# Kernel tuning notes

Measured on AMD Instinct MI355X. Metric: run time of the kernel, lower is better.

Reference implementation:

```python
import jax, jax.numpy as jnp
import numpy as np

N = 32768       # total nodes = NUM_GRAPHS * T
F_IN = 32       # num_features
HC = 64         # hidden_channels
HEADS = 4
E = 524288      # edges before self-loops
NUM_GRAPHS = 64 # == batch.max()+1 by construction
T = 512         # time steps per graph (N // NUM_GRAPHS)
OUT = 24        # output_size
NEG_SLOPE = 0.2 # PyG GATConv default


def gat_layer(x, src, dst, W, a_src, a_dst, b, n_nodes):
    """PyG GATConv (concat=True) with edge softmax over incoming edges."""
    H, C = a_src.shape
    h = (x @ W).reshape(n_nodes, H, C)                    # [N,H,C]
    alpha_src = jnp.sum(h * a_src, axis=-1)               # [N,H]
    alpha_dst = jnp.sum(h * a_dst, axis=-1)               # [N,H]
    e = jax.nn.leaky_relu(alpha_src[src] + alpha_dst[dst], NEG_SLOPE)  # [E,H]
    m = jax.ops.segment_max(e, dst, num_segments=n_nodes)
    e = jnp.exp(e - m[dst])
    s = jax.ops.segment_sum(e, dst, num_segments=n_nodes)
    alpha = e / (s[dst] + 1e-16)                          # [E,H]
    msg = h[src] * alpha[..., None]                       # [E,H,C]
    out = jax.ops.segment_sum(msg, dst, num_segments=n_nodes)  # [N,H,C]
    return out.reshape(n_nodes, H * C) + b


def gru_layer(x, Wih, Whh, bih, bhh):
    """torch nn.GRU single layer, batch_first input x: [B,T,Hin] -> ([B,T,H], h_T)."""
    Bsz = x.shape[0]
    H = Whh.shape[1]

    def step(h, xt):
        gi = xt @ Wih.T + bih
        gh = h @ Whh.T + bhh
        ir, iz, inn = jnp.split(gi, 3, axis=-1)
        hr, hz, hn = jnp.split(gh, 3, axis=-1)
        r = jax.nn.sigmoid(ir + hr)
        z = jax.nn.sigmoid(iz + hz)
        n = jnp.tanh(inn + r * hn)
        h_new = (1.0 - z) * n + z * h
        return h_new, h_new

    h0 = jnp.zeros((Bsz, H), x.dtype)
    hT, ys = jax.lax.scan(step, h0, jnp.swapaxes(x, 0, 1))
    return jnp.swapaxes(ys, 0, 1), hT


def setup_inputs() -> dict:
    key = jax.random.key(0)
    ks = jax.random.split(key, 24)
    sc = 0.1
    inp = {
        "x": jax.random.normal(ks[0], (N, F_IN), dtype=jnp.float32),
        "edge_index": jax.random.randint(ks[1], (2, E), 0, N, dtype=jnp.int32),
        "batch": jnp.repeat(jnp.arange(NUM_GRAPHS, dtype=jnp.int32), T),
        # GAT layer 1: F_IN -> HC x HEADS (concat)
        "W1": sc * jax.random.normal(ks[2], (F_IN, HEADS * HC), dtype=jnp.float32),
        "a_src1": sc * jax.random.normal(ks[3], (HEADS, HC), dtype=jnp.float32),
        "a_dst1": sc * jax.random.normal(ks[4], (HEADS, HC), dtype=jnp.float32),
        "b1": jnp.zeros((HEADS * HC,), dtype=jnp.float32),
        # GAT layer 2: HEADS*HC -> HC, 1 head
        "W2": sc * jax.random.normal(ks[5], (HEADS * HC, HC), dtype=jnp.float32),
        "a_src2": sc * jax.random.normal(ks[6], (1, HC), dtype=jnp.float32),
        "a_dst2": sc * jax.random.normal(ks[7], (1, HC), dtype=jnp.float32),
        "b2": jnp.zeros((HC,), dtype=jnp.float32),
        # GRU (2 layers, input_size == hidden_size == HC)
        "gru_Wih0": sc * jax.random.normal(ks[8], (3 * HC, HC), dtype=jnp.float32),
        "gru_Whh0": sc * jax.random.normal(ks[9], (3 * HC, HC), dtype=jnp.float32),
        "gru_bih0": jnp.zeros((3 * HC,), dtype=jnp.float32),
        "gru_bhh0": jnp.zeros((3 * HC,), dtype=jnp.float32),
        "gru_Wih1": sc * jax.random.normal(ks[10], (3 * HC, HC), dtype=jnp.float32),
        "gru_Whh1": sc * jax.random.normal(ks[11], (3 * HC, HC), dtype=jnp.float32),
        "gru_bih1": jnp.zeros((3 * HC,), dtype=jnp.float32),
        "gru_bhh1": jnp.zeros((3 * HC,), dtype=jnp.float32),
        # Linear head
        "Wl": sc * jax.random.normal(ks[12], (OUT, HC), dtype=jnp.float32),
        "bl": jnp.zeros((OUT,), dtype=jnp.float32),
    }
    return inp


def reference(x, edge_index, batch, W1, a_src1, a_dst1, b1, W2, a_src2, a_dst2, b2,
              gru_Wih0, gru_Whh0, gru_bih0, gru_bhh0,
              gru_Wih1, gru_Whh1, gru_bih1, gru_bhh1, Wl, bl):
    # PyG GATConv default add_self_loops=True
    loops = jnp.arange(N, dtype=edge_index.dtype)
    src = jnp.concatenate([edge_index[0], loops])
    dst = jnp.concatenate([edge_index[1], loops])

    h = jax.nn.elu(gat_layer(x, src, dst, W1, a_src1, a_dst1, b1, N))   # [N, HEADS*HC]
    h = jax.nn.elu(gat_layer(h, src, dst, W2, a_src2, a_dst2, b2, N))   # [N, HC]

    # batch is repeat(arange(NUM_GRAPHS), T) so batch.max()+1 == NUM_GRAPHS (static)
    seq = h.reshape(NUM_GRAPHS, T, HC)
    seq, _ = gru_layer(seq, gru_Wih0, gru_Whh0, gru_bih0, gru_bhh0)
    _, hT = gru_layer(seq, gru_Wih1, gru_Whh1, gru_bih1, gru_bhh1)      # [B, HC]
    return hT @ Wl.T + bl                                               # [B, OUT]
```

## Files before the change

kernel.cpp:

```cpp
#include <hip/hip_runtime.h>
#include <hip/hip_bf16.h>

#define N_NODES 32768
#define F_IN    32
#define HC      64
#define HEADS   4
#define NE      524288
#define NET     (NE + N_NODES)
#define NG      64
#define TT      512
#define OUTF    24

__device__ __forceinline__ float lrelu(float x){ return x > 0.f ? x : 0.2f*x; }
__device__ __forceinline__ float eluf (float x){ return x > 0.f ? x : __expf(x)-1.f; }
__device__ __forceinline__ float sigmf(float x){ return 1.f/(1.f+__expf(-x)); }
__device__ __forceinline__ float tanhfast(float x){ return 1.f - 2.f/(__expf(2.f*x)+1.f); }

__global__ __launch_bounds__(256) void k_deg(const int* __restrict__ ei,
                                             int* __restrict__ deg){
  int e = blockIdx.x*256 + threadIdx.x;
  int d = (e < NE) ? ei[NE+e] : (e - NE);
  atomicAdd(deg + d, 1);
}

__global__ __launch_bounds__(1024) void k_scan(const int* __restrict__ deg,
                                               int* __restrict__ rowptr){
  __shared__ int ps[1024];
  const int t = threadIdx.x;
  const int base = t*32;
  int local[32]; int s = 0;
  #pragma unroll
  for(int i=0;i<32;i++){ local[i]=deg[base+i]; s+=local[i]; }
  ps[t]=s; __syncthreads();
  for(int off=1; off<1024; off<<=1){
    int v = (t>=off) ? ps[t-off] : 0;
    __syncthreads();
    ps[t]+=v;
    __syncthreads();
  }
  int run = (t==0) ? 0 : ps[t-1];
  #pragma unroll
  for(int i=0;i<32;i++){ rowptr[base+i]=run; run+=local[i]; }
  if(t==1023) rowptr[N_NODES]=run;
}

__global__ __launch_bounds__(256) void k_fill(const int* __restrict__ ei,
                                              const int* __restrict__ rowptr,
                                              int* __restrict__ cur,
                                              int* __restrict__ col){
  int e = blockIdx.x*256 + threadIdx.x;
  int s, d;
  if(e < NE){ s = ei[e]; d = ei[NE+e]; } else { s = e-NE; d = s; }
  int pos = atomicAdd(cur + d, 1);
  col[rowptr[d] + pos] = s;
}

__global__ __launch_bounds__(256) void k_gemm1(const float* __restrict__ x,
                                               const float* __restrict__ W1,
                                               float* __restrict__ h1){
  __shared__ __align__(16) float xs[64*32];
  __shared__ __align__(16) float ws[32*256];
  const int tid = threadIdx.x;
  const int row0 = blockIdx.x*64;
  const float4* xg = (const float4*)(x + row0*F_IN);
  float4* xs4 = (float4*)xs;
  for(int i=tid;i<512;i+=256) xs4[i]=xg[i];
  const float4* wg=(const float4*)W1; float4* ws4=(float4*)ws;
  for(int i=tid;i<2048;i+=256) ws4[i]=wg[i];
  __syncthreads();
  float wc[32];
  #pragma unroll
  for(int k=0;k<32;k++) wc[k]=ws[k*256+tid];
  for(int r=0;r<64;r++){
    const float4* xr=(const float4*)(xs + r*32);
    float acc=0.f;
    #pragma unroll
    for(int k4=0;k4<8;k4++){
      float4 v=xr[k4];
      acc += v.x*wc[4*k4]+v.y*wc[4*k4+1]+v.z*wc[4*k4+2]+v.w*wc[4*k4+3];
    }
    h1[(row0+r)*256+tid]=acc;
  }
}

__global__ __launch_bounds__(256) void k_alpha1(const float* __restrict__ h1,
                                                const float* __restrict__ a_src,
                                                const float* __restrict__ a_dst,
                                                float* __restrict__ as1,
                                                float* __restrict__ ad1){
  int t = blockIdx.x*256 + threadIdx.x;
  int n = t>>2, h = t&3;
  const float4* hp=(const float4*)(h1 + n*256 + h*64);
  const float4* ap=(const float4*)(a_src + h*64);
  const float4* dp=(const float4*)(a_dst + h*64);
  float sa=0.f, sd=0.f;
  #pragma unroll
  for(int i=0;i<16;i++){
    float4 v=hp[i], a=ap[i], d=dp[i];
    sa += v.x*a.x+v.y*a.y+v.z*a.z+v.w*a.w;
    sd += v.x*d.x+v.y*d.y+v.z*d.z+v.w*d.w;
  }
  as1[t]=sa; ad1[t]=sd;
}

__global__ __launch_bounds__(256) void k_gat1(const int* __restrict__ rowptr,
                                              const int* __restrict__ col,
                                              const float* __restrict__ as1,
                                              const float* __restrict__ ad1,
                                              const float* __restrict__ h1,
                                              const float* __restrict__ b1,
                                              float* __restrict__ out1){
  const int node = blockIdx.x*4 + (threadIdx.x>>6);
  const int lane = threadIdx.x & 63;
  const int h    = lane>>4;
  const int beg = rowptr[node], end = rowptr[node+1];
  const float ad = ad1[node*4+h];
  float4 acc = make_float4(0.f,0.f,0.f,0.f);
  float s = 0.f;
  int j = beg;
  for(; j+1 < end; j += 2){
    int s0 = col[j], s1 = col[j+1];
    float w0 = __expf(lrelu(as1[s0*4+h] + ad));
    float w1 = __expf(lrelu(as1[s1*4+h] + ad));
    float4 v0 = *(const float4*)(h1 + s0*256 + lane*4);
    float4 v1 = *(const float4*)(h1 + s1*256 + lane*4);
    acc.x += w0*v0.x + w1*v1.x;
    acc.y += w0*v0.y + w1*v1.y;
    acc.z += w0*v0.z + w1*v1.z;
    acc.w += w0*v0.w + w1*v1.w;
    s += w0 + w1;
  }
  if(j < end){
    int s0 = col[j];
    float w0 = __expf(lrelu(as1[s0*4+h] + ad));
    float4 v0 = *(const float4*)(h1 + s0*256 + lane*4);
    acc.x += w0*v0.x; acc.y += w0*v0.y; acc.z += w0*v0.z; acc.w += w0*v0.w;
    s += w0;
  }
  const float inv = 1.f/(s + 1e-16f);
  float4 bb = ((const float4*)b1)[lane];
  float4 o;
  o.x = eluf(acc.x*inv + bb.x);
  o.y = eluf(acc.y*inv + bb.y);
  o.z = eluf(acc.z*inv + bb.z);
  o.w = eluf(acc.w*inv + bb.w);
  ((float4*)(out1 + node*256))[lane] = o;
}

__global__ __launch_bounds__(256) void k_gemm2(const float* __restrict__ in,
                                               const float* __restrict__ W2,
                                               float* __restrict__ h2){
  __shared__ __align__(16) float xs[64*256];
  const int tid=threadIdx.x;
  const int row0=blockIdx.x*64;
  const float4* xg=(const float4*)(in + row0*256);
  float4* xs4=(float4*)xs;
  for(int i=tid;i<4096;i+=256) xs4[i]=xg[i];
  __syncthreads();
  const int c0=(tid&15)*4;
  const int r0=(tid>>4)*4;
  float acc[4][4]={};
  for(int k=0;k<256;k+=4){
    float wv[4][4];
    #pragma unroll
    for(int i=0;i<4;i++){
      float4 w=*(const float4*)(W2+(k+i)*64+c0);
      wv[i][0]=w.x; wv[i][1]=w.y; wv[i][2]=w.z; wv[i][3]=w.w;
    }
    #pragma unroll
    for(int i=0;i<4;i++){
      float4 xv=*(const float4*)(xs+(r0+i)*256+k);
      #pragma unroll
      for(int j=0;j<4;j++)
        acc[i][j]+=xv.x*wv[0][j]+xv.y*wv[1][j]+xv.z*wv[2][j]+xv.w*wv[3][j];
    }
  }
  #pragma unroll
  for(int i=0;i<4;i++)
    *(float4*)(h2+(row0+r0+i)*64+c0)=make_float4(acc[i][0],acc[i][1],acc[i][2],acc[i][3]);
}

__global__ __launch_bounds__(256) void k_alpha2(const float* __restrict__ h2,
                                                const float* __restrict__ a_src,
                                                const float* __restrict__ a_dst,
                                                float* __restrict__ as2,
                                                float* __restrict__ ad2){
  int n = blockIdx.x*256 + threadIdx.x;
  const float4* hp=(const float4*)(h2+n*64);
  float sa=0.f, sd=0.f;
  #pragma unroll
  for(int i=0;i<16;i++){
    float4 v=hp[i];
    float4 a=((const float4*)a_src)[i];
    float4 d=((const float4*)a_dst)[i];
    sa+=v.x*a.x+v.y*a.y+v.z*a.z+v.w*a.w;
    sd+=v.x*d.x+v.y*d.y+v.z*d.z+v.w*d.w;
  }
  as2[n]=sa; ad2[n]=sd;
}

__global__ __launch_bounds__(256) void k_gat2(const int* __restrict__ rowptr,
                                              const int* __restrict__ col,
                                              const float* __restrict__ as2,
                                              const float* __restrict__ ad2,
                                              const float* __restrict__ h2,
                                              const float* __restrict__ b2,
                                              float* __restrict__ out2){
  const int node = blockIdx.x*4 + (threadIdx.x>>6);
  const int lane = threadIdx.x & 63;
  const int beg = rowptr[node], end = rowptr[node+1];
  const float ad = ad2[node];
  float acc = 0.f, s = 0.f;
  int j = beg;
  for(; j+1 < end; j += 2){
    int s0 = col[j], s1 = col[j+1];
    float w0 = __expf(lrelu(as2[s0] + ad));
    float w1 = __expf(lrelu(as2[s1] + ad));
    acc += w0*h2[s0*64+lane] + w1*h2[s1*64+lane];
    s += w0 + w1;
  }
  if(j < end){
    int s0 = col[j];
    float w0 = __expf(lrelu(as2[s0] + ad));
    acc += w0*h2[s0*64+lane];
    s += w0;
  }
  const float inv = 1.f/(s + 1e-16f);
  out2[node*64+lane] = eluf(acc*inv + b2[lane]);
}

__global__ __launch_bounds__(256) void k_gemm_gi(const float* __restrict__ in,
                                                 const float* __restrict__ Wih,
                                                 const float* __restrict__ bih,
                                                 float* __restrict__ gi){
  __shared__ __align__(16) float xs[64*64];
  __shared__ float wT[64*192];
  const int tid=threadIdx.x;
  const int row0=blockIdx.x*64;
  const float4* xg=(const float4*)(in+row0*64);
  float4* xs4=(float4*)xs;
  for(int i=tid;i<1024;i+=256) xs4[i]=xg[i];
  for(int i=tid;i<12288;i+=256){ wT[(i&63)*192+(i>>6)] = Wih[i]; }
  __syncthreads();
  if(tid<192){
    float wr[64];
    #pragma unroll
    for(int k=0;k<64;k++) wr[k]=wT[k*192+tid];
    const float bj=bih[tid];
    for(int r=0;r<64;r++){
      float acc=bj;
      const float4* xr=(const float4*)(xs+r*64);
      #pragma unroll
      for(int k4=0;k4<16;k4++){
        float4 v=xr[k4];
        acc+=v.x*wr[4*k4]+v.y*wr[4*k4+1]+v.z*wr[4*k4+2]+v.w*wr[4*k4+3];
      }
      gi[(row0+r)*192+tid]=acc;
    }
  }
}

__global__ __launch_bounds__(576) void k_gruF(const float* __restrict__ gi1,
                                              const float* __restrict__ Whh0,
                                              const float* __restrict__ bhh0,
                                              const float* __restrict__ Wih1,
                                              const float* __restrict__ bih1,
                                              const float* __restrict__ Whh1,
                                              const float* __restrict__ bhh1,
                                              const float* __restrict__ Wl,
                                              const float* __restrict__ bl,
                                              float* __restrict__ fout){
  __shared__ __align__(16) float h1s[64];
  __shared__ __align__(16) float h2s[64];
  __shared__ float gh1s[192];
  __shared__ float gi2s[192];
  __shared__ float gh2s[192];
  __shared__ __align__(16) float gic[64*192];
  const int tid  = threadIdx.x;
  const int lane = tid & 63;
  const int w    = tid >> 6;
  const int crew = tid/192;
  const int row  = tid - crew*192;
  const int b    = blockIdx.x;
  const float* gib = gi1 + (size_t)b*TT*192;
  float4* gic4 = (float4*)gic;

  float* dst       = (crew==0) ? gh1s : (crew==1) ? gi2s : gh2s;
  const float* bb  = (crew==0) ? bhh0 : (crew==1) ? bih1 : bhh1;
  const float* hsrc= (crew==2) ? h2s  : h1s;

  float wr[64];
  {
    const float* Ws[3] = { Whh0, Wih1, Whh1 };
    for(int c=0;c<3;c++){
      const float4* g = (const float4*)Ws[c];
      for(int l=tid;l<3072;l+=576) gic4[l] = g[l];
      __syncthreads();
      if(crew==c){
        const float4* wl = (const float4*)(gic + row*64);
        #pragma unroll
        for(int k4=0;k4<16;k4++){
          float4 v = wl[k4];
          wr[4*k4]=v.x; wr[4*k4+1]=v.y; wr[4*k4+2]=v.z; wr[4*k4+3]=v.w;
        }
      }
      __syncthreads();
    }
  }
  const float bias = bb[row];
  if(tid < 64){ h1s[tid]=0.f; h2s[tid]=0.f; }
  __syncthreads();

#define MATVEC() do{ \
    float a0=bias, a1=0.f, a2=0.f, a3=0.f; \
    const float4* h4p = (const float4*)hsrc; \
    _Pragma("unroll") \
    for(int k4=0;k4<16;k4++){ \
      float4 h4 = h4p[k4]; \
      a0 = fmaf(h4.x, wr[4*k4  ], a0); \
      a1 = fmaf(h4.y, wr[4*k4+1], a1); \
      a2 = fmaf(h4.z, wr[4*k4+2], a2); \
      a3 = fmaf(h4.w, wr[4*k4+3], a3); \
    } \
    dst[row] = (a0+a1)+(a2+a3); \
  }while(0)

  for(int c=0;c<8;c++){
    const float4* g4 = (const float4*)gib + (size_t)c*3072;
    for(int l=tid; l<3072; l+=576) gic4[l] = g4[l];
    __syncthreads();
    for(int j=0;j<64;j++){
      const int i = c*64 + j;
      MATVEC();
      __syncthreads();
      if(w == 0){
        float r = sigmf(gic[j*192+lane]     + gh1s[lane]);
        float z = sigmf(gic[j*192+64+lane]  + gh1s[64+lane]);
        float n = tanhfast(gic[j*192+128+lane] + r*gh1s[128+lane]);
        h1s[lane] = (1.f-z)*n + z*h1s[lane];
      } else if(w == 3){
        if(i >= 1){
          float r = sigmf(gi2s[lane]     + gh2s[lane]);
          float z = sigmf(gi2s[64+lane]  + gh2s[64+lane]);
          float n = tanhfast(gi2s[128+lane] + r*gh2s[128+lane]);
          h2s[lane] = (1.f-z)*n + z*h2s[lane];
        }
      }
      __syncthreads();
    }
  }
  MATVEC();
  __syncthreads();
  if(w == 3){
    float r = sigmf(gi2s[lane]     + gh2s[lane]);
    float z = sigmf(gi2s[64+lane]  + gh2s[64+lane]);
    float n = tanhfast(gi2s[128+lane] + r*gh2s[128+lane]);
    h2s[lane] = (1.f-z)*n + z*h2s[lane];
  }
  __syncthreads();
#undef MATVEC

  if(tid < 24){
    float acc = bl[tid];
    const float4* wl4 = (const float4*)(Wl + tid*64);
    #pragma unroll
    for(int k4=0;k4<16;k4++){
      float4 h4 = *(const float4*)(h2s + 4*k4);
      float4 w4 = wl4[k4];
      acc += h4.x*w4.x + h4.y*w4.y + h4.z*w4.z + h4.w*w4.w;
    }
    fout[b*24+tid] = acc;
  }
}

extern "C" void kernel_launch(void* const* d_in, const int* in_sizes, int n_in,
                              void* d_out, int out_size, void* d_ws, size_t ws_size,
                              hipStream_t stream){
  const float* x     =(const float*)d_in[0];
  const int*   ei    =(const int*  )d_in[1];
  const float* W1    =(const float*)d_in[3];
  const float* a_src1=(const float*)d_in[4];
  const float* a_dst1=(const float*)d_in[5];
  const float* b1    =(const float*)d_in[6];
  const float* W2    =(const float*)d_in[7];
  const float* a_src2=(const float*)d_in[8];
  const float* a_dst2=(const float*)d_in[9];
  const float* b2    =(const float*)d_in[10];
  const float* Wih0  =(const float*)d_in[11];
  const float* Whh0  =(const float*)d_in[12];
  const float* bih0  =(const float*)d_in[13];
  const float* bhh0  =(const float*)d_in[14];
  const float* Wih1  =(const float*)d_in[15];
  const float* Whh1  =(const float*)d_in[16];
  const float* bih1  =(const float*)d_in[17];
  const float* bhh1  =(const float*)d_in[18];
  const float* Wl    =(const float*)d_in[19];
  const float* bl    =(const float*)d_in[20];

  float* ws   = (float*)d_ws;
  float* h1   = ws;
  float* gi   = ws;
  float* out1 = ws + 8388608;
  float* out2 = out1;
  float* h2   = ws + 16777216;
  float* as1  = ws + 18874368;
  float* ad1  = as1 + 131072;
  float* as2  = ad1 + 131072;
  float* ad2  = as2 + 32768;
  int* rowptr = (int*)(ad2 + 32768);
  int* deg    = rowptr + 32800;
  int* cur    = deg + 32768;
  int* col    = cur + 32768;
  float* fo   = (float*)d_out;

  hipMemsetAsync(deg, 0, 2*32768*sizeof(int), stream);

  k_deg  <<<2176,256,0,stream>>>(ei,deg);
  k_scan <<<1  ,1024,0,stream>>>(deg,rowptr);
  k_fill <<<2176,256,0,stream>>>(ei,rowptr,cur,col);

  k_gemm1 <<<512 ,256,0,stream>>>(x,W1,h1);
  k_alpha1<<<512 ,256,0,stream>>>(h1,a_src1,a_dst1,as1,ad1);
  k_gat1  <<<8192,256,0,stream>>>(rowptr,col,as1,ad1,h1,b1,out1);
  k_gemm2 <<<512 ,256,0,stream>>>(out1,W2,h2);
  k_alpha2<<<128 ,256,0,stream>>>(h2,a_src2,a_dst2,as2,ad2);
  k_gat2  <<<8192,256,0,stream>>>(rowptr,col,as2,ad2,h2,b2,out2);
  k_gemm_gi<<<512,256,0,stream>>>(out2,Wih0,bih0,gi);
  k_gruF  <<<64 ,576,0,stream>>>(gi,Whh0,bhh0,Wih1,bih1,Whh1,bhh1,Wl,bl,fo);
  (void)in_sizes; (void)n_in; (void)out_size; (void)ws_size;
}
```

Measured before the change: 863.3 us.

## Shrink GRU recurrence block to 320 threads with two matvec rows per thread

The fused two-layer GRU kernel is relaunched with 5 waves instead of 9. Each thread now computes two output rows of the per-step matvecs. Threads 0-191 handle the layer-1 hidden projection and the layer-2 input projection, and the rest split the layer-2 hidden projection two rows apiece. Weights are staged through shared memory with a transpose so each thread can pick up its column. The aim is to cut barrier and scheduling cost in the latency-bound 512-step serial loop, at the price of doubled FMA chains per thread and more registers.

```diff
diff --git a/kernel.cpp b/kernel.cpp
--- a/kernel.cpp
+++ b/kernel.cpp
@@ -260,7 +260,7 @@
   }
 }
 
-__global__ __launch_bounds__(576) void k_gruF(const float* __restrict__ gi1,
+__global__ __launch_bounds__(320) void k_gruH(const float* __restrict__ gi1,
                                               const float* __restrict__ Whh0,
                                               const float* __restrict__ bhh0,
                                               const float* __restrict__ Wih1,
@@ -279,55 +279,67 @@
   const int tid  = threadIdx.x;
   const int lane = tid & 63;
   const int w    = tid >> 6;
-  const int crew = tid/192;
-  const int row  = tid - crew*192;
   const int b    = blockIdx.x;
   const float* gib = gi1 + (size_t)b*TT*192;
   float4* gic4 = (float4*)gic;
 
-  float* dst       = (crew==0) ? gh1s : (crew==1) ? gi2s : gh2s;
-  const float* bb  = (crew==0) ? bhh0 : (crew==1) ? bih1 : bhh1;
-  const float* hsrc= (crew==2) ? h2s  : h1s;
-
-  float wr[64];
-  {
-    const float* Ws[3] = { Whh0, Wih1, Whh1 };
-    for(int c=0;c<3;c++){
-      const float4* g = (const float4*)Ws[c];
-      for(int l=tid;l<3072;l+=576) gic4[l] = g[l];
-      __syncthreads();
-      if(crew==c){
-        const float4* wl = (const float4*)(gic + row*64);
-        #pragma unroll
-        for(int k4=0;k4<16;k4++){
-          float4 v = wl[k4];
-          wr[4*k4]=v.x; wr[4*k4+1]=v.y; wr[4*k4+2]=v.z; wr[4*k4+3]=v.w;
-        }
-      }
-      __syncthreads();
-    }
-  }
-  const float bias = bb[row];
+  const bool cA  = (tid < 192);
+  const int  u0  = tid - 192;
+  const int  u   = (!cA && u0 < 96) ? u0 : 95;
+  const bool act = cA || (u0 < 96);
+  const int rowA = cA ? tid : 2*u;
+  const int rowB = cA ? tid : 2*u+1;
+  const float* hsrc = cA ? h1s : h2s;
+
+  float wA[64], wB[64];
+  for(int i=tid;i<12288;i+=320) gic[(i&63)*192+(i>>6)] = Whh0[i];
+  __syncthreads();
+  if(cA){
+    #pragma unroll
+    for(int k=0;k<64;k++) wA[k] = gic[k*192+rowA];
+  }
+  __syncthreads();
+  for(int i=tid;i<12288;i+=320) gic[(i&63)*192+(i>>6)] = Wih1[i];
+  __syncthreads();
+  if(cA){
+    #pragma unroll
+    for(int k=0;k<64;k++) wB[k] = gic[k*192+rowA];
+  }
+  __syncthreads();
+  for(int i=tid;i<12288;i+=320) gic[(i&63)*192+(i>>6)] = Whh1[i];
+  __syncthreads();
+  if(!cA){
+    #pragma unroll
+    for(int k=0;k<64;k++){ wA[k] = gic[k*192+rowA]; wB[k] = gic[k*192+rowB]; }
+  }
+  __syncthreads();
+  const float bA = cA ? bhh0[rowA] : bhh1[rowA];
+  const float bB = cA ? bih1[rowA] : bhh1[rowB];
+
   if(tid < 64){ h1s[tid]=0.f; h2s[tid]=0.f; }
   __syncthreads();
 
 #define MATVEC() do{ \
-    float a0=bias, a1=0.f, a2=0.f, a3=0.f; \
+    float a0=bA, a1=0.f, a2=0.f, a3=0.f; \
+    float c0=bB, c1=0.f, c2=0.f, c3=0.f; \
     const float4* h4p = (const float4*)hsrc; \
     _Pragma("unroll") \
     for(int k4=0;k4<16;k4++){ \
       float4 h4 = h4p[k4]; \
-      a0 = fmaf(h4.x, wr[4*k4  ], a0); \
-      a1 = fmaf(h4.y, wr[4*k4+1], a1); \
-      a2 = fmaf(h4.z, wr[4*k4+2], a2); \
-      a3 = fmaf(h4.w, wr[4*k4+3], a3); \
+      a0 = fmaf(h4.x, wA[4*k4  ], a0);  c0 = fmaf(h4.x, wB[4*k4  ], c0); \
+      a1 = fmaf(h4.y, wA[4*k4+1], a1);  c1 = fmaf(h4.y, wB[4*k4+1], c1); \
+      a2 = fmaf(h4.z, wA[4*k4+2], a2);  c2 = fmaf(h4.z, wB[4*k4+2], c2); \
+      a3 = fmaf(h4.w, wA[4*k4+3], a3);  c3 = fmaf(h4.w, wB[4*k4+3], c3); \
     } \
-    dst[row] = (a0+a1)+(a2+a3); \
+    if(act){ \
+      if(cA){ gh1s[rowA] = (a0+a1)+(a2+a3); gi2s[rowA] = (c0+c1)+(c2+c3); } \
+      else  { gh2s[rowA] = (a0+a1)+(a2+a3); gh2s[rowB] = (c0+c1)+(c2+c3); } \
+    } \
   }while(0)
 
   for(int c=0;c<8;c++){
     const float4* g4 = (const float4*)gib + (size_t)c*3072;
-    for(int l=tid; l<3072; l+=576) gic4[l] = g4[l];
+    for(int l=tid; l<3072; l+=320) gic4[l] = g4[l];
     __syncthreads();
     for(int j=0;j<64;j++){
       const int i = c*64 + j;
@@ -426,6 +438,6 @@
   k_alpha2<<<128 ,256,0,stream>>>(h2,a_src2,a_dst2,as2,ad2);
   k_gat2  <<<8192,256,0,stream>>>(rowptr,col,as2,ad2,h2,b2,out2);
   k_gemm_gi<<<512,256,0,stream>>>(out2,Wih0,bih0,gi);
-  k_gruF  <<<64 ,576,0,stream>>>(gi,Whh0,bhh0,Wih1,bih1,Whh1,bhh1,Wl,bl,fo);
+  k_gruH  <<<64 ,320,0,stream>>>(gi,Whh0,bhh0,Wih1,bih1,Whh1,bhh1,Wl,bl,fo);
   (void)in_sizes; (void)n_in; (void)out_size; (void)ws_size;
 }
```

Result: slower. 932.1 us (+8.0%).
